# Performance work log

Hardware: AMD Instinct MI355X
Metric: run time of the kernel (lower is better)

Reference implementation:

```python
import jax, jax.numpy as jnp
import numpy as np

N_KV_HEADS = 8
MAX_CONTEXT = 8192
HEAD_DIM = 128  # dim // n_heads = 4096 // 32
N_NEW = 16


def setup_inputs() -> dict:
    key = jax.random.key(0)
    k1, k2, k3, k4, k5 = jax.random.split(key, 5)
    pos_ids = jnp.sort(jax.random.randint(k1, (N_NEW,), 0, MAX_CONTEXT, dtype=jnp.int64))
    k = jax.random.normal(k2, (1, N_KV_HEADS, N_NEW, HEAD_DIM), dtype=jnp.float32)
    v = jax.random.normal(k3, (1, N_KV_HEADS, N_NEW, HEAD_DIM), dtype=jnp.float32)
    k_cache = jax.random.normal(k4, (1, N_KV_HEADS, MAX_CONTEXT, HEAD_DIM), dtype=jnp.float32)
    v_cache = jax.random.normal(k5, (1, N_KV_HEADS, MAX_CONTEXT, HEAD_DIM), dtype=jnp.float32)
    return {"pos_ids": pos_ids, "k": k, "v": v, "k_cache": k_cache, "v_cache": v_cache}


def reference(pos_ids, k, v, k_cache, v_cache):
    # Functional equivalent of: clone cache, then cache[:, :, pos_ids, :] = new.
    # jnp .at[].set on the seq axis produces a fresh (copied) buffer, matching
    # the torch clone-then-scatter semantics.
    kout = k_cache.at[:, :, pos_ids, :].set(k)
    vout = v_cache.at[:, :, pos_ids, :].set(v)
    return (kout, vout)
```

## Files before the change

kernel.cpp:

```cpp
#include <hip/hip_runtime.h>


#define NNEW 16

__global__ __launch_bounds__(256) void kv_update_kernel(
    const int* __restrict__ pos,
    const float4* __restrict__ knew,
    const float4* __restrict__ vnew,
    const float4* __restrict__ kcache,
    const float4* __restrict__ vcache,
    float4* __restrict__ out)
{
    const unsigned int i = blockIdx.x * 256u + threadIdx.x;

    const unsigned int is_v = i >> 21;
    const unsigned int j = i & ((1u << 21) - 1u);
    const unsigned int h  = j >> 18;
    const int          s  = (int)((j >> 5) & 8191u);
    const unsigned int d4 = j & 31u;

    int match = -1;
#pragma unroll
    for (int n = 0; n < NNEW; ++n) {
        if (pos[n] == s) match = n;
    }

    float4 val;
    if (match >= 0) {
        const float4* __restrict__ src = is_v ? vnew : knew;
        val = src[(h * NNEW + (unsigned)match) * 32u + d4];
    } else {
        const float4* __restrict__ src = is_v ? vcache : kcache;
        val = src[j];
    }
    out[i] = val;
}

extern "C" void kernel_launch(void* const* d_in, const int* in_sizes, int n_in,
                              void* d_out, int out_size, void* d_ws, size_t ws_size,
                              hipStream_t stream) {
    const int*    pos    = (const int*)   d_in[0];
    const float4* knew   = (const float4*)d_in[1];
    const float4* vnew   = (const float4*)d_in[2];
    const float4* kcache = (const float4*)d_in[3];
    const float4* vcache = (const float4*)d_in[4];
    float4*       out    = (float4*)d_out;

    const unsigned int nblocks = (1u << 22) / 256u;
    kv_update_kernel<<<nblocks, 256, 0, stream>>>(pos, knew, vnew, kcache, vcache, out);
}
```

Baseline: 119.3 us.

## Split KV update into plain streaming copy plus small scatter kernel

Result: slower. 128.3 us (+7.5%).

```diff
diff --git a/kernel.cpp b/kernel.cpp
--- a/kernel.cpp
+++ b/kernel.cpp
@@ -3,49 +3,56 @@
 
 #define NNEW 16
 
-__global__ __launch_bounds__(256) void kv_update_kernel(
-    const int* __restrict__ pos,
-    const float4* __restrict__ knew,
-    const float4* __restrict__ vnew,
-    const float4* __restrict__ kcache,
-    const float4* __restrict__ vcache,
-    float4* __restrict__ out)
+typedef float f32x4 __attribute__((ext_vector_type(4)));
+
+__global__ __launch_bounds__(256) void kv_copy_kernel(
+    const f32x4* __restrict__ kcache,
+    const f32x4* __restrict__ vcache,
+    f32x4* __restrict__ out)
 {
     const unsigned int i = blockIdx.x * 256u + threadIdx.x;
+    const unsigned int j = i & ((1u << 21) - 1u);
+    const f32x4* __restrict__ src = (i >> 21) ? vcache : kcache;
+    f32x4 val = __builtin_nontemporal_load(&src[j]);
+    __builtin_nontemporal_store(val, &out[i]);
+}
 
-    const unsigned int is_v = i >> 21;
-    const unsigned int j = i & ((1u << 21) - 1u);
-    const unsigned int h  = j >> 18;
-    const int          s  = (int)((j >> 5) & 8191u);
-    const unsigned int d4 = j & 31u;
+__global__ __launch_bounds__(256) void kv_scatter_kernel(
+    const int* __restrict__ pos,
+    const f32x4* __restrict__ knew,
+    const f32x4* __restrict__ vnew,
+    f32x4* __restrict__ out)
+{
+    const unsigned int t  = blockIdx.x * 256u + threadIdx.x;
+    const unsigned int d4 = t & 31u;
+    const unsigned int n  = (t >> 5) & 15u;
+    const unsigned int h  = (t >> 9) & 7u;
+    const unsigned int c  = t >> 12;
 
-    int match = -1;
+    const int s = pos[n];
+
+    bool skip = false;
 #pragma unroll
-    for (int n = 0; n < NNEW; ++n) {
-        if (pos[n] == s) match = n;
+    for (int m = 0; m < NNEW; ++m) {
+        if (m > (int)n && pos[m] == s) skip = true;
     }
+    if (skip) return;
 
-    float4 val;
-    if (match >= 0) {
-        const float4* __restrict__ src = is_v ? vnew : knew;
-        val = src[(h * NNEW + (unsigned)match) * 32u + d4];
-    } else {
-        const float4* __restrict__ src = is_v ? vcache : kcache;
-        val = src[j];
-    }
-    out[i] = val;
+    const f32x4* __restrict__ src = c ? vnew : knew;
+    out[(c << 21) + (h << 18) + ((unsigned)s << 5) + d4] =
+        src[(h * NNEW + n) * 32u + d4];
 }
 
 extern "C" void kernel_launch(void* const* d_in, const int* in_sizes, int n_in,
                               void* d_out, int out_size, void* d_ws, size_t ws_size,
                               hipStream_t stream) {
-    const int*    pos    = (const int*)   d_in[0];
-    const float4* knew   = (const float4*)d_in[1];
-    const float4* vnew   = (const float4*)d_in[2];
-    const float4* kcache = (const float4*)d_in[3];
-    const float4* vcache = (const float4*)d_in[4];
-    float4*       out    = (float4*)d_out;
+    const int*   pos    = (const int*)  d_in[0];
+    const f32x4* knew   = (const f32x4*)d_in[1];
+    const f32x4* vnew   = (const f32x4*)d_in[2];
+    const f32x4* kcache = (const f32x4*)d_in[3];
+    const f32x4* vcache = (const f32x4*)d_in[4];
+    f32x4*       out    = (f32x4*)d_out;
 
-    const unsigned int nblocks = (1u << 22) / 256u;
-    kv_update_kernel<<<nblocks, 256, 0, stream>>>(pos, knew, vnew, kcache, vcache, out);
+    kv_copy_kernel<<<(1u << 22) / 256u, 256, 0, stream>>>(kcache, vcache, out);
+    kv_scatter_kernel<<<8192 / 256, 256, 0, stream>>>(pos, knew, vnew, out);
 }
```
